# Kernel tuning notes

Measured on AMD Instinct MI355X. Metric: run time of the kernel, lower is better.

Reference implementation:

```python
import jax, jax.numpy as jnp
import numpy as np

ALPHA = 0.1

def ewma(y, alpha=ALPHA):
    # y: [B, T, D]; x_ewma[0] = y[0], x_ewma[t] = alpha*y[t] + (1-alpha)*x_ewma[t-1]
    y_t = jnp.swapaxes(y, 0, 1)  # [T, B, D]
    def step(carry, xt):
        c = alpha * xt + (1.0 - alpha) * carry
        return c, c
    _, out = jax.lax.scan(step, y_t[0], y_t[1:])  # [T-1, B, D]
    out = jnp.concatenate([y_t[:1], out], axis=0)  # [T, B, D]
    return jnp.swapaxes(out, 0, 1)


def setup_inputs() -> dict:
    key = jax.random.key(0)
    k1, k2, k3, k4, k5 = jax.random.split(key, 5)
    B, C, T, D = 32, 32, 2048, 512
    x = jax.random.normal(k1, (B, C, T), dtype=jnp.float32)
    W_ve = jax.random.normal(k2, (D, C), dtype=jnp.float32) * (1.0 / np.sqrt(C))
    b_ve = jax.random.normal(k3, (D,), dtype=jnp.float32) * 0.01
    W_lin = jax.random.normal(k4, (D, D), dtype=jnp.float32) * (1.0 / np.sqrt(D))
    b_lin = jax.random.normal(k5, (D,), dtype=jnp.float32) * 0.01
    return {"x": x, "W_ve": W_ve, "b_ve": b_ve, "W_lin": W_lin, "b_lin": b_lin}


def reference(x, W_ve, b_ve, W_lin, b_lin):
    # x: [B, C, T] -> [B, T, C]
    xt = jnp.transpose(x, (0, 2, 1))
    B, T, C = xt.shape
    # first-difference with leading zero row
    x_diff = jnp.concatenate(
        [jnp.zeros((B, 1, C), dtype=xt.dtype), xt[:, 1:, :] - xt[:, :-1, :]], axis=1
    )
    # value embedding: Linear(C -> D)
    x_emb = jnp.einsum("btc,dc->btd", x_diff, W_ve) + b_ve
    # bidirectional EWMA smoothing
    x_lr = ewma(x_emb)
    x_rl = jnp.flip(ewma(jnp.flip(x_emb, axis=1)), axis=1)
    x_smooth = (x_lr + x_rl) * 0.5
    # output projection: Linear(D -> D)
    return jnp.einsum("btd,ed->bte", x_smooth, W_lin) + b_lin
```

## Files before the change

kernel.cpp:

```cpp
#include <hip/hip_runtime.h>

constexpr int B = 32, C = 32, T = 2048, D = 512;
constexpr float ALPHA = 0.1f;
constexpr float BETA  = 0.9f;
constexpr float LOG2_BETA = -0.15200309344504997f;

typedef float floatx4 __attribute__((ext_vector_type(4)));

constexpr int CHUNK = 128;
constexpr int SUB   = 16;
constexpr int HALO  = 128;
constexpr int WIN   = CHUNK + 2 * HALO + 2;
constexpr int PAD   = WIN + 1;

__global__ __launch_bounds__(256) void combine_weights(
    const float* __restrict__ W_ve, const float* __restrict__ b_ve,
    const float* __restrict__ W_lin, const float* __restrict__ b_lin,
    float* __restrict__ W_comb, float* __restrict__ b_comb) {
  int e  = blockIdx.x;
  int c  = threadIdx.x & 31;
  int ds = threadIdx.x >> 5;
  float acc = 0.f, accb = 0.f;
#pragma unroll 4
  for (int i = 0; i < 64; ++i) {
    int d = ds * 64 + i;
    float wl = W_lin[e * D + d];
    acc  += wl * W_ve[d * C + c];
    accb += wl * b_ve[d];
  }
  __shared__ float red[8][33];
  __shared__ float redb[8];
  red[ds][c] = acc;
  if (c == 0) redb[ds] = accb;
  __syncthreads();
  if (ds == 0) {
    float ssum = 0.f;
#pragma unroll
    for (int k = 0; k < 8; ++k) ssum += red[k][c];
    W_comb[e * C + c] = ssum;
    if (c == 0) {
      float sb = 0.f;
#pragma unroll
      for (int k = 0; k < 8; ++k) sb += redb[k];
      b_comb[e] = sb + b_lin[e];
    }
  }
}

__global__ __launch_bounds__(256) void fused_main(
    const float* __restrict__ x, const float* __restrict__ W_comb,
    const float* __restrict__ b_comb, float* __restrict__ out) {
  int b  = blockIdx.y;
  int t0 = blockIdx.x * CHUNK;
  int wlo = t0 - HALO - 1;

  __shared__ float xl[C * PAD];
  const float* xb = x + (size_t)b * C * T;

  for (int idx = threadIdx.x; idx < C * WIN; idx += 256) {
    int c  = idx / WIN;
    int tt = idx - c * WIN;
    int t  = wlo + tt;
    t = min(max(t, 0), T - 1);
    xl[c * PAD + tt] = xb[c * T + t];
  }

  int li   = threadIdx.x & 127;
  int half = threadIdx.x >> 7;
  int e0   = li * 4;
  float w[4][C], bias[4];
#pragma unroll
  for (int j = 0; j < 4; ++j) {
    const float4* wr = (const float4*)(W_comb + (e0 + j) * C);
#pragma unroll
    for (int c4 = 0; c4 < C / 4; ++c4) {
      float4 wv = wr[c4];
      w[j][c4 * 4 + 0] = wv.x;
      w[j][c4 * 4 + 1] = wv.y;
      w[j][c4 * 4 + 2] = wv.z;
      w[j][c4 * 4 + 3] = wv.w;
    }
    bias[j] = b_comb[e0 + j];
  }
  __syncthreads();

  int c   = threadIdx.x & 31;
  int sub = threadIdx.x >> 5;
  int ts  = t0 + sub * SUB;
  int te  = ts + SUB - 1;
  const float* xc = xl + c * PAD - wlo;

#define DD(t) (xc[(t)] - xc[(t) - 1])

  float fc = 0.f, bc = 0.f;
#pragma unroll 8
  for (int k = HALO; k >= 1; --k) {
    float df = DD(ts - k);
    float db = DD(te + k);
    fc = ALPHA * df + BETA * fc;
    bc = ALPHA * db + BETA * bc;
  }

  float lr[SUB];
#pragma unroll
  for (int i = 0; i < SUB; ++i) {
    fc = ALPHA * DD(ts + i) + BETA * fc;
    lr[i] = fc;
  }

  float dlast = xb[c * T + (T - 1)] - xb[c * T + (T - 2)];
  float fcor  = exp2f((float)(T - te) * LOG2_BETA);
#pragma unroll
  for (int i = SUB - 1; i >= 0; --i) {
    bc = ALPHA * DD(ts + i) + BETA * bc;
    lr[i] = 0.5f * (lr[i] + bc + fcor * dlast);
    fcor *= BETA;
  }
#undef DD

  __syncthreads();

  float* sbuf = xl;
  {
    int tbase = sub * SUB;
#pragma unroll
    for (int i = 0; i < SUB; ++i) sbuf[(tbase + i) * C + c] = lr[i];
  }
  __syncthreads();

  const float* srow = sbuf + half * (CHUNK / 2) * C;
  float* orow = out + ((size_t)b * T + t0 + half * (CHUNK / 2)) * D + e0;

  for (int t = 0; t < CHUNK / 2; ++t) {
    float a[4], a2[4];
#pragma unroll
    for (int j = 0; j < 4; ++j) { a[j] = bias[j]; a2[j] = 0.f; }
    const float4* sr4 = (const float4*)(srow + t * C);
#pragma unroll
    for (int c4 = 0; c4 < C / 4; ++c4) {
      float4 sv = sr4[c4];
      int cc = c4 * 4;
#pragma unroll
      for (int j = 0; j < 4; ++j) {
        a[j]  += sv.x * w[j][cc + 0];
        a2[j] += sv.y * w[j][cc + 1];
        a[j]  += sv.z * w[j][cc + 2];
        a2[j] += sv.w * w[j][cc + 3];
      }
    }
    floatx4 o;
    o.x = a[0] + a2[0];
    o.y = a[1] + a2[1];
    o.z = a[2] + a2[2];
    o.w = a[3] + a2[3];
    __builtin_nontemporal_store(o, (floatx4*)orow);
    orow += D;
  }
}

extern "C" void kernel_launch(void* const* d_in, const int* in_sizes, int n_in,
                              void* d_out, int out_size, void* d_ws, size_t ws_size,
                              hipStream_t stream) {
  const float* x     = (const float*)d_in[0];
  const float* W_ve  = (const float*)d_in[1];
  const float* b_ve  = (const float*)d_in[2];
  const float* W_lin = (const float*)d_in[3];
  const float* b_lin = (const float*)d_in[4];
  float* out = (float*)d_out;

  float* W_comb = (float*)d_ws;
  float* b_comb = W_comb + (size_t)D * C;

  combine_weights<<<D, 256, 0, stream>>>(W_ve, b_ve, W_lin, b_lin, W_comb, b_comb);
  fused_main<<<dim3(T / CHUNK, B), 256, 0, stream>>>(x, W_comb, b_comb, out);
}
```

Baseline: 181.9 us.

## Replace per-subchunk halo recurrence with shared-memory chunked EWMA carry scan

```diff
diff --git a/kernel.cpp b/kernel.cpp
--- a/kernel.cpp
+++ b/kernel.cpp
@@ -4,14 +4,16 @@
 constexpr float ALPHA = 0.1f;
 constexpr float BETA  = 0.9f;
 constexpr float LOG2_BETA = -0.15200309344504997f;
+constexpr float BETA16    = 0.18530201888518410f;
 
 typedef float floatx4 __attribute__((ext_vector_type(4)));
 
 constexpr int CHUNK = 128;
 constexpr int SUB   = 16;
-constexpr int HALO  = 128;
-constexpr int WIN   = CHUNK + 2 * HALO + 2;
-constexpr int PAD   = WIN + 1;
+constexpr int NSUB  = CHUNK / SUB;
+constexpr int LEAD  = 132;
+constexpr int WIN   = LEAD + CHUNK + 128;
+constexpr int PAD   = WIN + 2;
 
 __global__ __launch_bounds__(256) void combine_weights(
     const float* __restrict__ W_ve, const float* __restrict__ b_ve,
@@ -50,19 +52,36 @@
 __global__ __launch_bounds__(256) void fused_main(
     const float* __restrict__ x, const float* __restrict__ W_comb,
     const float* __restrict__ b_comb, float* __restrict__ out) {
-  int b  = blockIdx.y;
-  int t0 = blockIdx.x * CHUNK;
-  int wlo = t0 - HALO - 1;
+  int b   = blockIdx.y;
+  int t0  = blockIdx.x * CHUNK;
+  int wlo = t0 - LEAD;
 
   __shared__ float xl[C * PAD];
+  __shared__ float Lf[2][NSUB][C];
+  __shared__ float Lb[2][NSUB][C];
   const float* xb = x + (size_t)b * C * T;
 
-  for (int idx = threadIdx.x; idx < C * WIN; idx += 256) {
-    int c  = idx / WIN;
-    int tt = idx - c * WIN;
-    int t  = wlo + tt;
-    t = min(max(t, 0), T - 1);
-    xl[c * PAD + tt] = xb[c * T + t];
+  int c   = threadIdx.x & 31;
+  int sub = threadIdx.x >> 5;
+
+  float dlast = xb[c * T + (T - 1)] - xb[c * T + (T - 2)];
+
+  if (wlo >= 0 && wlo + WIN <= T) {
+    for (int idx = threadIdx.x; idx < C * (WIN / 4); idx += 256) {
+      int cc = idx / (WIN / 4);
+      int q  = idx - cc * (WIN / 4);
+      float4 v   = *(const float4*)(xb + cc * T + wlo + 4 * q);
+      float* dst = xl + cc * PAD + 4 * q;
+      ((float2*)dst)[0] = make_float2(v.x, v.y);
+      ((float2*)dst)[1] = make_float2(v.z, v.w);
+    }
+  } else {
+    for (int idx = threadIdx.x; idx < C * WIN; idx += 256) {
+      int cc = idx / WIN;
+      int tt = idx - cc * WIN;
+      int t  = min(max(wlo + tt, 0), T - 1);
+      xl[cc * PAD + tt] = xb[cc * T + t];
+    }
   }
 
   int li   = threadIdx.x & 127;
@@ -84,41 +103,58 @@
   }
   __syncthreads();
 
-  int c   = threadIdx.x & 31;
-  int sub = threadIdx.x >> 5;
-  int ts  = t0 + sub * SUB;
-  int te  = ts + SUB - 1;
+  int ts = t0 + sub * SUB;
   const float* xc = xl + c * PAD - wlo;
-
 #define DD(t) (xc[(t)] - xc[(t) - 1])
 
-  float fc = 0.f, bc = 0.f;
-#pragma unroll 8
-  for (int k = HALO; k >= 1; --k) {
-    float df = DD(ts - k);
-    float db = DD(te + k);
-    fc = ALPHA * df + BETA * fc;
-    bc = ALPHA * db + BETA * bc;
-  }
-
-  float lr[SUB];
+  int ha = t0 - 128   + sub * SUB;
+  int ba = t0 + CHUNK + sub * SUB;
+  float fh = 0.f, bh = 0.f;
 #pragma unroll
   for (int i = 0; i < SUB; ++i) {
-    fc = ALPHA * DD(ts + i) + BETA * fc;
-    lr[i] = fc;
-  }
-
-  float dlast = xb[c * T + (T - 1)] - xb[c * T + (T - 2)];
-  float fcor  = exp2f((float)(T - te) * LOG2_BETA);
+    fh = ALPHA * DD(ha + i)           + BETA * fh;
+    bh = ALPHA * DD(ba + SUB - 1 - i) + BETA * bh;
+  }
+  float lr[SUB], rl[SUB];
+  float fm = 0.f, bm = 0.f;
+#pragma unroll
+  for (int i = 0; i < SUB; ++i) {
+    fm = ALPHA * DD(ts + i) + BETA * fm;
+    lr[i] = fm;
+    bm = ALPHA * DD(ts + SUB - 1 - i) + BETA * bm;
+    rl[SUB - 1 - i] = bm;
+  }
+  Lf[0][sub][c] = fh;
+  Lf[1][sub][c] = lr[SUB - 1];
+  Lb[0][sub][c] = bh;
+  Lb[1][sub][c] = rl[0];
+  __syncthreads();
+#undef DD
+
+  float Cc = 0.f, Bc = 0.f;
+#pragma unroll
+  for (int h = 0; h < NSUB; ++h) {
+    Cc = BETA16 * Cc + Lf[0][h][c];
+    Bc = BETA16 * Bc + Lb[0][NSUB - 1 - h][c];
+  }
+#pragma unroll
+  for (int j = 0; j < NSUB - 1; ++j) {
+    float cn = BETA16 * Cc + Lf[1][j][c];
+    float bn = BETA16 * Bc + Lb[1][NSUB - 1 - j][c];
+    Cc = (j < sub)            ? cn : Cc;
+    Bc = (NSUB - 1 - j > sub) ? bn : Bc;
+  }
+  float f = BETA * Cc;
+#pragma unroll
+  for (int i = 0; i < SUB; ++i) { lr[i] += f; f *= BETA; }
+  float g = BETA * Bc;
+  float e = exp2f((float)(T - ts - (SUB - 1)) * LOG2_BETA);
 #pragma unroll
   for (int i = SUB - 1; i >= 0; --i) {
-    bc = ALPHA * DD(ts + i) + BETA * bc;
-    lr[i] = 0.5f * (lr[i] + bc + fcor * dlast);
-    fcor *= BETA;
-  }
-#undef DD
-
-  __syncthreads();
+    lr[i] = 0.5f * (lr[i] + (rl[i] + g) + e * dlast);
+    g *= BETA;
+    e *= BETA;
+  }
 
   float* sbuf = xl;
   {
@@ -131,6 +167,7 @@
   const float* srow = sbuf + half * (CHUNK / 2) * C;
   float* orow = out + ((size_t)b * T + t0 + half * (CHUNK / 2)) * D + e0;
 
+#pragma unroll 2
   for (int t = 0; t < CHUNK / 2; ++t) {
     float a[4], a2[4];
 #pragma unroll
@@ -153,8 +190,7 @@
     o.y = a[1] + a2[1];
     o.z = a[2] + a2[2];
     o.w = a[3] + a2[3];
-    __builtin_nontemporal_store(o, (floatx4*)orow);
-    orow += D;
+    __builtin_nontemporal_store(o, (floatx4*)(orow + (size_t)t * D));
   }
 }
 
```

After: 177.3 us. 2.6% less time.
